# Performance work log

Hardware: AMD Instinct MI355X
Metric: run time of the kernel (lower is better)

Reference implementation:

```python
import jax, jax.numpy as jnp
import numpy as np

N_HEAD = 16
N_KV_HEADS = 4
N_REP = 4
HEAD_DIM = 128
N_EMBD = 2048
EPS = 1e-5
ROPE_BASE = 10000.0


def setup_inputs() -> dict:
    key = jax.random.key(0)
    ks = jax.random.split(key, 5)
    B, T, C = 2, 2048, N_EMBD
    s = 0.02
    return {
        "x": jax.random.normal(ks[0], (B, T, C), dtype=jnp.float32),
        "wq": jax.random.normal(ks[1], (C, N_HEAD * HEAD_DIM), dtype=jnp.float32) * s,
        "wk": jax.random.normal(ks[2], (C, N_KV_HEADS * HEAD_DIM), dtype=jnp.float32) * s,
        "wv": jax.random.normal(ks[3], (C, N_KV_HEADS * HEAD_DIM), dtype=jnp.float32) * s,
        "wc": jax.random.normal(ks[4], (C, C), dtype=jnp.float32) * s,
        "q_norm_w": jnp.ones((HEAD_DIM,), dtype=jnp.float32),
        "k_norm_w": jnp.ones((HEAD_DIM,), dtype=jnp.float32),
    }


def _rmsnorm(x, w):
    # norm in fp32, scale by weight (matches RMSNorm.forward)
    xf = x.astype(jnp.float32)
    rms = jax.lax.rsqrt(jnp.mean(xf * xf, axis=-1, keepdims=True) + EPS)
    return (xf * rms).astype(x.dtype) * w


def _rope(x, cos, sin):
    # x: [B,T,H,D]; cos/sin: [T, D//2]; interleaved even/odd rotation
    xf = x.astype(jnp.float32)
    xe = xf[..., 0::2]
    xo = xf[..., 1::2]
    c = cos[None, :, None, :]
    s = sin[None, :, None, :]
    ye = xe * c - xo * s
    yo = xe * s + xo * c
    y = jnp.stack((ye, yo), axis=-1).reshape(x.shape)
    return y.astype(x.dtype)


def reference(x, wq, wk, wv, wc, q_norm_w, k_norm_w):
    B, T, C = x.shape
    q = (x @ wq).reshape(B, T, N_HEAD, HEAD_DIM)
    k = (x @ wk).reshape(B, T, N_KV_HEADS, HEAD_DIM)
    v = (x @ wv).reshape(B, T, N_KV_HEADS, HEAD_DIM)

    q = _rmsnorm(q, q_norm_w)
    k = _rmsnorm(k, k_norm_w)

    inv_freq = 1.0 / (ROPE_BASE ** (jnp.arange(0, HEAD_DIM, 2, dtype=jnp.float32) / HEAD_DIM))
    theta = jnp.arange(T, dtype=jnp.float32)[:, None] * inv_freq[None, :]  # [T, D//2]
    cos, sin = jnp.cos(theta), jnp.sin(theta)
    q = _rope(q, cos, sin)
    k = _rope(k, cos, sin)

    # GQA: repeat kv heads (repeat_kv with n_rep)
    k = jnp.repeat(k, N_REP, axis=2)  # [B,T,H,D]
    v = jnp.repeat(v, N_REP, axis=2)

    scale = 1.0 / jnp.sqrt(jnp.float32(HEAD_DIM))
    scores = jnp.einsum("bthd,bshd->bhts", q, k) * scale  # [B,H,T,S]
    causal = jnp.tril(jnp.ones((T, T), dtype=bool))
    scores = jnp.where(causal[None, None], scores, jnp.finfo(scores.dtype).min)
    attn = jax.nn.softmax(scores, axis=-1)
    y = jnp.einsum("bhts,bshd->bthd", attn, v).reshape(B, T, C)
    return y @ wc
```

## Files before the change

### kernel.cpp

```cpp
#include <hip/hip_runtime.h>
#include <hip/hip_bf16.h>
#include <cstdint>
#include <cstddef>

using bf16 = __hip_bfloat16;
typedef __attribute__((ext_vector_type(8))) short short8;
typedef __attribute__((ext_vector_type(4))) float f32x4;
typedef __attribute__((ext_vector_type(16))) float f32x16;

#define T_SEQ 2048
#define NHEAD 16
#define NKV 4
#define HD 128
#define CE 2048

__device__ __forceinline__ void gl_lds16(const void* g, void* l) {
  __builtin_amdgcn_global_load_lds(
      (const __attribute__((address_space(1))) unsigned int*)g,
      (__attribute__((address_space(3))) unsigned int*)l, 16, 0, 0);
}

__device__ __forceinline__ unsigned int cvtpk_bf16(float lo, float hi) {
  unsigned int r;
  asm("v_cvt_pk_bf16_f32 %0, %1, %2" : "=v"(r) : "v"(lo), "v"(hi));
  return r;
}

__device__ __forceinline__ void plswap(unsigned int& x, unsigned int& y, int hi) {
#if __has_builtin(__builtin_amdgcn_permlane32_swap)
  auto r = __builtin_amdgcn_permlane32_swap(x, y, false, false);
  x = r[0];
  y = r[1];
#else
  unsigned int xp = (unsigned int)__shfl_xor((int)x, 32);
  unsigned int yp = (unsigned int)__shfl_xor((int)y, 32);
  unsigned int nx = hi ? yp : x;
  unsigned int ny = hi ? y : xp;
  x = nx;
  y = ny;
#endif
}

__global__ void __launch_bounds__(256) cvt_bf16(const float* __restrict__ in,
                                                bf16* __restrict__ out, int n4) {
  const int i = blockIdx.x * blockDim.x + threadIdx.x;
  if (i >= n4) return;
  const float4 v = ((const float4*)in)[i];
  bf16 b0 = __float2bfloat16(v.x), b1 = __float2bfloat16(v.y),
       b2 = __float2bfloat16(v.z), b3 = __float2bfloat16(v.w);
  ushort4 u;
  u.x = *(const unsigned short*)&b0; u.y = *(const unsigned short*)&b1;
  u.z = *(const unsigned short*)&b2; u.w = *(const unsigned short*)&b3;
  ((ushort4*)out)[i] = u;
}

__global__ void __launch_bounds__(256) transpose_cvt(const float* __restrict__ W,
                                                     bf16* __restrict__ Wt, int N) {
  __shared__ float tile[32][33];
  const int tx = threadIdx.x & 31, ty = threadIdx.x >> 5;
  const int bx = blockIdx.x, by = blockIdx.y;
#pragma unroll
  for (int i = 0; i < 4; i++) {
    const int r = by * 32 + ty + i * 8;
    tile[ty + i * 8][tx] = W[(size_t)r * N + bx * 32 + tx];
  }
  __syncthreads();
#pragma unroll
  for (int i = 0; i < 4; i++) {
    const int n = bx * 32 + ty + i * 8;
    Wt[(size_t)n * 2048 + by * 32 + tx] = __float2bfloat16(tile[tx][ty + i * 8]);
  }
}

template <int BM, int BN, int WM, int WN, bool OBF>
__global__ void __launch_bounds__(512, 2)
gemm8i(const bf16* __restrict__ A, const bf16* __restrict__ Bt,
       void* __restrict__ Cv, int M, int N, int K) {
  constexpr int AWS = BM / 2 / WM;
  constexpr int BWS = BN / 2 / WN;
  constexpr int MH = AWS / 16;
  constexpr int NH = BWS / 16;
  constexpr int AH = BM / 128;
  constexpr int BH = BN / 128;
  constexpr int G = 2 * AH + BH;
  __shared__ bf16 smA[2][BM * 64];
  __shared__ bf16 smB[2][BN * 64];

  const int tid = threadIdx.x, lane = tid & 63, wid = tid >> 6;
  const int l15 = lane & 15, l4 = lane >> 4;
  const int wr = wid / WN, wc = wid % WN;

  const int nwg = gridDim.x;
  const int q = nwg >> 3, r = nwg & 7;
  const int xcd = blockIdx.x & 7, lin = blockIdx.x >> 3;
  const int wg = (xcd < r ? xcd * (q + 1) : r * (q + 1) + (xcd - r) * q) + lin;
  const int gw = N / BN;
  const int by = wg / gw, bx = wg % gw;
  const int row0 = by * BM, col0 = bx * BN;
  const int NT = K >> 6;
  const int NI = NT >> 1;

  const bf16* Ag = A + (size_t)row0 * K;
  const bf16* Bg = Bt + (size_t)col0 * K;

  auto stA = [&](int t, int h, int pb) {
    const int k0 = t << 6;
#pragma unroll
    for (int j = 0; j < AH; j++) {
      const int c = (h * AH + j) * 512 + tid;
      const int rowi = c >> 3;
      gl_lds16(Ag + (size_t)rowi * K + k0 + (((c & 7) ^ (rowi & 7)) << 3),
               (void*)(&smA[pb][(size_t)c << 3]));
    }
  };
  auto stB = [&](int t, int h, int pb) {
    const int k0 = t << 6;
#pragma unroll
    for (int j = 0; j < BH; j++) {
      const int c = (h * BH + j) * 512 + tid;
      const int rowi = c >> 3;
      gl_lds16(Bg + (size_t)rowi * K + k0 + (((c & 7) ^ (rowi & 7)) << 3),
               (void*)(&smB[pb][(size_t)c << 3]));
    }
  };
  auto rdA = [&](const bf16* sA, int mh, short8 (&dst)[MH][2]) {
#pragma unroll
    for (int i = 0; i < MH; i++) {
      const int rowl = mh * (BM / 2) + wr * AWS + i * 16 + l15;
#pragma unroll
      for (int kk = 0; kk < 2; kk++)
        dst[i][kk] = *(const short8*)(sA + rowl * 64 +
                                      ((((kk << 2) | l4) ^ (rowl & 7)) << 3));
    }
  };
  auto rdB = [&](const bf16* sB, int nh, short8 (&dst)[NH][2]) {
#pragma unroll
    for (int j = 0; j < NH; j++) {
      const int rowl = nh * (BN / 2) + wc * BWS + j * 16 + l15;
#pragma unroll
      for (int kk = 0; kk < 2; kk++)
        dst[j][kk] = *(const short8*)(sB + rowl * 64 +
                                      ((((kk << 2) | l4) ^ (rowl & 7)) << 3));
    }
  };

  f32x4 acc[2][2][MH][NH];
#pragma unroll
  for (int mh = 0; mh < 2; mh++)
#pragma unroll
    for (int nh = 0; nh < 2; nh++)
#pragma unroll
      for (int i = 0; i < MH; i++)
#pragma unroll
        for (int j = 0; j < NH; j++) acc[mh][nh][i][j] = (f32x4){0.f, 0.f, 0.f, 0.f};

  auto mmq = [&](short8 (&a)[MH][2], short8 (&b)[NH][2], f32x4 (&ac)[MH][NH]) {
    __builtin_amdgcn_s_setprio(1);
#pragma unroll
    for (int i = 0; i < MH; i++)
#pragma unroll
      for (int j = 0; j < NH; j++)
#pragma unroll
        for (int kk = 0; kk < 2; kk++)
          ac[i][j] = __builtin_amdgcn_mfma_f32_16x16x32_bf16(a[i][kk], b[j][kk],
                                                             ac[i][j], 0, 0, 0);
    __builtin_amdgcn_s_setprio(0);
  };

  short8 a0[MH][2], a1[MH][2], b0[NH][2], b1[NH][2];

#define LGKM0_SB                                            \
  asm volatile("s_waitcnt lgkmcnt(0)" ::: "memory");        \
  __builtin_amdgcn_sched_barrier(0);
#define GATE_G                                              \
  asm volatile("s_waitcnt vmcnt(%0)" ::"i"(G) : "memory");

  stA(0, 0, 0); stB(0, 0, 0); stA(0, 1, 0); stB(0, 1, 0);
  stA(1, 0, 1); stB(1, 0, 1); stA(1, 1, 1);
  GATE_G
  __builtin_amdgcn_s_barrier();

  for (int i = 0; i < NI - 1; ++i) {
    const int u = 2 * i, v = u + 1;
    stB(v, 1, 1);
    rdA(smA[0], 0, a0); rdB(smB[0], 0, b0);
    __builtin_amdgcn_s_barrier();
    LGKM0_SB
    mmq(a0, b0, acc[0][0]);
    __builtin_amdgcn_s_barrier();
    stA(u + 2, 0, 0);
    rdA(smA[0], 1, a1);
    __builtin_amdgcn_s_barrier();
    LGKM0_SB
    mmq(a1, b0, acc[1][0]);
    __builtin_amdgcn_s_barrier();
    stB(u + 2, 0, 0);
    rdB(smB[0], 1, b1);
    __builtin_amdgcn_s_barrier();
    LGKM0_SB
    mmq(a1, b1, acc[1][1]);
    __builtin_amdgcn_s_barrier();
    stA(u + 2, 1, 0);
    mmq(a0, b1, acc[0][1]);
    GATE_G
    __builtin_amdgcn_s_barrier();
    stB(u + 2, 1, 0);
    rdA(smA[1], 0, a0); rdB(smB[1], 0, b0);
    __builtin_amdgcn_s_barrier();
    LGKM0_SB
    mmq(a0, b0, acc[0][0]);
    __builtin_amdgcn_s_barrier();
    stA(v + 2, 0, 1);
    rdA(smA[1], 1, a1);
    __builtin_amdgcn_s_barrier();
    LGKM0_SB
    mmq(a1, b0, acc[1][0]);
    __builtin_amdgcn_s_barrier();
    stB(v + 2, 0, 1);
    rdB(smB[1], 1, b1);
    __builtin_amdgcn_s_barrier();
    LGKM0_SB
    mmq(a1, b1, acc[1][1]);
    __builtin_amdgcn_s_barrier();
    stA(v + 2, 1, 1);
    mmq(a0, b1, acc[0][1]);
    GATE_G
    __builtin_amdgcn_s_barrier();
  }

  {
    stB(NT - 1, 1, 1);
    rdA(smA[0], 0, a0); rdB(smB[0], 0, b0);
    __builtin_amdgcn_s_barrier();
    LGKM0_SB
    mmq(a0, b0, acc[0][0]);
    __builtin_amdgcn_s_barrier();
    rdA(smA[0], 1, a1);
    __builtin_amdgcn_s_barrier();
    LGKM0_SB
    mmq(a1, b0, acc[1][0]);
    __builtin_amdgcn_s_barrier();
    rdB(smB[0], 1, b1);
    __builtin_amdgcn_s_barrier();
    LGKM0_SB
    mmq(a1, b1, acc[1][1]);
    __builtin_amdgcn_s_barrier();
    mmq(a0, b1, acc[0][1]);
    asm volatile("s_waitcnt vmcnt(0)" ::: "memory");
    __builtin_amdgcn_s_barrier();
    rdA(smA[1], 0, a0); rdB(smB[1], 0, b0);
    __builtin_amdgcn_s_barrier();
    LGKM0_SB
    mmq(a0, b0, acc[0][0]);
    __builtin_amdgcn_s_barrier();
    rdA(smA[1], 1, a1);
    __builtin_amdgcn_s_barrier();
    LGKM0_SB
    mmq(a1, b0, acc[1][0]);
    __builtin_amdgcn_s_barrier();
    rdB(smB[1], 1, b1);
    __builtin_amdgcn_s_barrier();
    LGKM0_SB
    mmq(a1, b1, acc[1][1]);
    mmq(a0, b1, acc[0][1]);
  }

#pragma unroll
  for (int mh = 0; mh < 2; mh++)
#pragma unroll
    for (int nh = 0; nh < 2; nh++)
#pragma unroll
      for (int i = 0; i < MH; i++)
#pragma unroll
        for (int j = 0; j < NH; j++)
#pragma unroll
          for (int rr = 0; rr < 4; rr++) {
            const size_t row = row0 + mh * (BM / 2) + wr * AWS + i * 16 + l4 * 4 + rr;
            const size_t col = col0 + nh * (BN / 2) + wc * BWS + j * 16 + l15;
            if constexpr (OBF)
              ((bf16*)Cv)[row * N + col] = __float2bfloat16(acc[mh][nh][i][j][rr]);
            else
              ((float*)Cv)[row * N + col] = acc[mh][nh][i][j][rr];
          }
#undef LGKM0_SB
#undef GATE_G
}

__global__ void __launch_bounds__(256) qkv_post(const bf16* __restrict__ QKV,
                                                const float* __restrict__ qw,
                                                const float* __restrict__ kw,
                                                bf16* __restrict__ Qo,
                                                bf16* __restrict__ Ko,
                                                bf16* __restrict__ Vto) {
  const int g = blockIdx.x * 4 + (threadIdx.x >> 6);
  const int lane = threadIdx.x & 63;
  const int hh = g % 24;
  const int bt = g / 24;
  const int b = bt >> 11, t = bt & (T_SEQ - 1);
  int off;
  if (hh < 16) off = hh * 128;
  else if (hh < 20) off = 2048 + (hh - 16) * 128;
  else off = 2560 + (hh - 20) * 128;
  const ushort2 xr = *(const ushort2*)(QKV + (size_t)bt * 3072 + off + lane * 2);
  const float xx = __bfloat162float(*(const bf16*)&xr.x);
  const float xy = __bfloat162float(*(const bf16*)&xr.y);
  if (hh < 20) {
    float ss = xx * xx + xy * xy;
    ss += __shfl_xor(ss, 1);  ss += __shfl_xor(ss, 2);  ss += __shfl_xor(ss, 4);
    ss += __shfl_xor(ss, 8);  ss += __shfl_xor(ss, 16); ss += __shfl_xor(ss, 32);
    const float rms = rsqrtf(ss * (1.0f / 128.0f) + 1e-5f);
    const float* w = (hh < 16) ? qw : kw;
    const float x0 = xx * rms * w[lane * 2];
    const float x1 = xy * rms * w[lane * 2 + 1];
    const float inv = exp2f((float)lane * (-13.287712379549449f / 64.0f));
    const float th = (float)t * inv;
    const float sn = sinf(th), cs = cosf(th);
    const float y0 = x0 * cs - x1 * sn;
    const float y1 = x0 * sn + x1 * cs;
    const bf16 o0 = __float2bfloat16(y0), o1 = __float2bfloat16(y1);
    if (hh < 16) {
      bf16* d = Qo + ((size_t)(b * NHEAD + hh) * T_SEQ + t) * HD + lane * 2;
      d[0] = o0; d[1] = o1;
    } else {
      bf16* d = Ko + ((size_t)(b * NKV + (hh - 16)) * T_SEQ + t) * HD + lane * 2;
      d[0] = o0; d[1] = o1;
    }
  } else {
    bf16* d = Vto + ((size_t)(b * NKV + (hh - 20)) * HD + lane * 2) * T_SEQ + t;
    d[0] = __float2bfloat16(xx);
    d[T_SEQ] = __float2bfloat16(xy);
  }
}

__global__ void __launch_bounds__(256, 2) attn_fwd(const bf16* __restrict__ Q,
                                                   const bf16* __restrict__ K,
                                                   const bf16* __restrict__ Vt,
                                                   bf16* __restrict__ Y) {
  __shared__ bf16 smK[128 * 128];
  __shared__ bf16 smV[128 * 128];

  const int bid = blockIdx.x;
  const int p = bid & 255, sdx = bid >> 8;
  const int bh = p & 31;
  const int jh = p >> 5;
  const int jq = sdx ? (15 - jh) : jh;
  const int h = bh & (NHEAD - 1), b = bh >> 4;
  const int bkv = b * NKV + (h >> 2);

  const int tid = threadIdx.x, wid = tid >> 6, lane = tid & 63;
  const int l31 = lane & 31, hi = lane >> 5;
  const int q0w = jq * 128 + wid * 32;

  const bf16* Kb = K + (size_t)bkv * T_SEQ * HD;
  const bf16* Vb = Vt + (size_t)bkv * HD * T_SEQ;

  const bf16* Qrow = Q + ((size_t)bh * T_SEQ + q0w + l31) * HD + hi * 8;
  short8 qf[8];
#pragma unroll
  for (int ds = 0; ds < 8; ds++) qf[ds] = *(const short8*)(Qrow + ds * 16);

  f32x16 o[4];
#pragma unroll
  for (int d = 0; d < 4; d++) o[d] = (f32x16)(0.f);
  float mrun = -INFINITY, lrun = 0.f;

  constexpr float CL = 0.08838834764831845f * 1.44269504088896340736f;
  const int trow = tid >> 4, tslot = tid & 15;

  for (int t = 0; t <= jq; t++) {
    const int k0 = t * 128;
    __syncthreads();
#pragma unroll
    for (int i = 0; i < 8; i++) {
      const int row = i * 16 + trow;
      const int ss = (tslot ^ (row & 15)) * 8;
      gl_lds16(Kb + (size_t)(k0 + row) * HD + ss, (void*)((char*)smK + i * 4096 + wid * 1024));
      gl_lds16(Vb + (size_t)row * T_SEQ + k0 + ss, (void*)((char*)smV + i * 4096 + wid * 1024));
    }
    __syncthreads();

    const bool lastt = (t == jq);
    const int glim = lastt ? wid : 3;

    f32x16 sg[4];
#pragma unroll
    for (int g = 0; g < 4; g++) {
      if (g > glim) continue;
      f32x16 acc = (f32x16)(0.f);
#pragma unroll
      for (int ds = 0; ds < 8; ds++) {
        const int row = g * 32 + l31;
        const short8 kf = *(const short8*)(smK + (size_t)row * 128 +
                                           (((ds << 1) | hi) ^ (row & 15)) * 8);
        acc = __builtin_amdgcn_mfma_f32_32x32x16_bf16(kf, qf[ds], acc, 0, 0, 0);
      }
      sg[g] = acc;
    }
    float tmax = -INFINITY;
#pragma unroll
    for (int g = 0; g < 4; g++) {
      if (g > glim) continue;
      if (lastt && g == wid) {
#pragma unroll
        for (int r = 0; r < 16; r++) {
          const int kr = (r & 3) + 8 * (r >> 2) + (hi << 2);
          if (kr > l31) sg[g][r] = -INFINITY;
        }
      }
#pragma unroll
      for (int r = 0; r < 16; r++) tmax = fmaxf(tmax, sg[g][r]);
    }
    tmax = fmaxf(tmax, __shfl_xor(tmax, 32));
    const float mnew = fmaxf(mrun, tmax);
    const float f = exp2f((mrun - mnew) * CL);
    mrun = mnew;
    lrun *= f;
#pragma unroll
    for (int d = 0; d < 4; d++)
#pragma unroll
      for (int r = 0; r < 16; r++) o[d][r] *= f;

    float lsum = 0.f;
#pragma unroll
    for (int g = 0; g < 4; g++) {
      if (g > glim) continue;
      float pp[16];
      float s0 = 0.f, s1 = 0.f;
#pragma unroll
      for (int r = 0; r < 16; r++) pp[r] = exp2f((sg[g][r] - mnew) * CL);
#pragma unroll
      for (int r = 0; r < 8; r++) { s0 += pp[2 * r]; s1 += pp[2 * r + 1]; }
      lsum += s0 + s1;

      unsigned int w0 = cvtpk_bf16(pp[0], pp[1]),  w2 = cvtpk_bf16(pp[4], pp[5]);
      unsigned int w1 = cvtpk_bf16(pp[2], pp[3]),  w3 = cvtpk_bf16(pp[6], pp[7]);
      unsigned int w4 = cvtpk_bf16(pp[8], pp[9]),  w6 = cvtpk_bf16(pp[12], pp[13]);
      unsigned int w5 = cvtpk_bf16(pp[10], pp[11]), w7 = cvtpk_bf16(pp[14], pp[15]);
      plswap(w0, w2, hi); plswap(w1, w3, hi);
      plswap(w4, w6, hi); plswap(w5, w7, hi);
      union { unsigned int u[4]; short8 s8; } pa0, pa1;
      pa0.u[0] = w0; pa0.u[1] = w1; pa0.u[2] = w2; pa0.u[3] = w3;
      pa1.u[0] = w4; pa1.u[1] = w5; pa1.u[2] = w6; pa1.u[3] = w7;

#pragma unroll
      for (int d = 0; d < 4; d++) {
        const int row = d * 32 + l31;
        const int ks0 = g * 2, ks1 = g * 2 + 1;
        const short8 vf0 = *(const short8*)(smV + (size_t)row * 128 +
                                            (((ks0 << 1) | hi) ^ (row & 15)) * 8);
        const short8 vf1 = *(const short8*)(smV + (size_t)row * 128 +
                                            (((ks1 << 1) | hi) ^ (row & 15)) * 8);
        o[d] = __builtin_amdgcn_mfma_f32_32x32x16_bf16(vf0, pa0.s8, o[d], 0, 0, 0);
        o[d] = __builtin_amdgcn_mfma_f32_32x32x16_bf16(vf1, pa1.s8, o[d], 0, 0, 0);
      }
    }
    lrun += lsum + __shfl_xor(lsum, 32);
  }

  const float inv = 1.0f / lrun;
  bf16* yrow = Y + ((size_t)(b * T_SEQ + q0w + l31)) * CE + h * HD;
#pragma unroll
  for (int d = 0; d < 4; d++) {
#pragma unroll
    for (int rg = 0; rg < 4; rg++) {
      ushort4 u;
      bf16 e0 = __float2bfloat16(o[d][rg * 4 + 0] * inv);
      bf16 e1 = __float2bfloat16(o[d][rg * 4 + 1] * inv);
      bf16 e2 = __float2bfloat16(o[d][rg * 4 + 2] * inv);
      bf16 e3 = __float2bfloat16(o[d][rg * 4 + 3] * inv);
      u.x = *(const unsigned short*)&e0; u.y = *(const unsigned short*)&e1;
      u.z = *(const unsigned short*)&e2; u.w = *(const unsigned short*)&e3;
      *(ushort4*)(yrow + d * 32 + rg * 8 + (hi << 2)) = u;
    }
  }
}

extern "C" void kernel_launch(void* const* d_in, const int* in_sizes, int n_in,
                              void* d_out, int out_size, void* d_ws, size_t ws_size,
                              hipStream_t stream) {
  const float* x   = (const float*)d_in[0];
  const float* wq  = (const float*)d_in[1];
  const float* wk  = (const float*)d_in[2];
  const float* wv  = (const float*)d_in[3];
  const float* wc  = (const float*)d_in[4];
  const float* qnw = (const float*)d_in[5];
  const float* knw = (const float*)d_in[6];
  float* out = (float*)d_out;

  char* ws = (char*)d_ws;
  bf16*  xb    = (bf16*)(ws);
  bf16*  wqkvt = (bf16*)(ws + 16777216);
  bf16*  wct   = (bf16*)(ws + 29360128);
  bf16*  qkv   = (bf16*)(ws + 37748736);
  bf16*  Qb    = (bf16*)(ws + 88080384);
  bf16*  Kb    = (bf16*)(ws + 104857600);
  bf16*  Vtb   = (bf16*)(ws + 109051904);
  bf16*  yb    = (bf16*)(ws + 113246208);

  cvt_bf16<<<8192, 256, 0, stream>>>(x, xb, 2097152);
  transpose_cvt<<<dim3(64, 64), 256, 0, stream>>>(wq, wqkvt, 2048);
  transpose_cvt<<<dim3(16, 64), 256, 0, stream>>>(wk, wqkvt + (size_t)2048 * 2048, 512);
  transpose_cvt<<<dim3(16, 64), 256, 0, stream>>>(wv, wqkvt + (size_t)2560 * 2048, 512);
  transpose_cvt<<<dim3(64, 64), 256, 0, stream>>>(wc, wct, 2048);
  gemm8i<256, 256, 2, 4, true><<<192, 512, 0, stream>>>(xb, wqkvt, qkv, 4096, 3072, 2048);
  qkv_post<<<24576, 256, 0, stream>>>(qkv, qnw, knw, Qb, Kb, Vtb);
  attn_fwd<<<512, 256, 0, stream>>>(Qb, Kb, Vtb, yb);
  gemm8i<128, 256, 2, 4, false><<<256, 512, 0, stream>>>(yb, wct, out, 4096, 2048, 2048);
}
```

Baseline: 228.2 us.

## Double-buffer 64-key KV tiles in attention with async prefetch and lazy rescale

The attention kernel now works on 64-key K/V tiles held in two LDS buffers. The next-but-one tile is prefetched with global_load_lds while the current tile is computed, which replaces the load, barrier, compute pattern that left global latency exposed. It also skips the output rescale unless the running max grows past a threshold, and raises wave priority around the MFMA blocks. The cost is more barriers per key, and the conditional rescale relies on the fp32 accumulator having enough headroom.

Result: slower. 237.9 us (+4.3%).

```diff
diff --git a/kernel.cpp b/kernel.cpp
--- a/kernel.cpp
+++ b/kernel.cpp
@@ -336,8 +336,8 @@
                                                    const bf16* __restrict__ K,
                                                    const bf16* __restrict__ Vt,
                                                    bf16* __restrict__ Y) {
-  __shared__ bf16 smK[128 * 128];
-  __shared__ bf16 smV[128 * 128];
+  __shared__ bf16 smK[2][64 * 128];
+  __shared__ bf16 smV[2][128 * 64];
 
   const int bid = blockIdx.x;
   const int p = bid & 255, sdx = bid >> 8;
@@ -359,75 +359,89 @@
 #pragma unroll
   for (int ds = 0; ds < 8; ds++) qf[ds] = *(const short8*)(Qrow + ds * 16);
 
+  auto stage = [&](int t, int pb) {
+    const int k0 = t * 64;
+#pragma unroll
+    for (int j = 0; j < 4; j++) {
+      const int c = j * 256 + tid;
+      const int rK = c >> 4, sK = c & 15;
+      gl_lds16(Kb + (size_t)(k0 + rK) * HD + ((sK ^ (rK & 15)) << 3),
+               (void*)((char*)smK[pb] + ((size_t)c << 4)));
+      const int rV = c >> 3, sV = c & 7;
+      gl_lds16(Vb + (size_t)rV * T_SEQ + k0 + ((sV ^ (rV & 7)) << 3),
+               (void*)((char*)smV[pb] + ((size_t)c << 4)));
+    }
+  };
+
   f32x16 o[4];
 #pragma unroll
   for (int d = 0; d < 4; d++) o[d] = (f32x16)(0.f);
   float mrun = -INFINITY, lrun = 0.f;
 
   constexpr float CL = 0.08838834764831845f * 1.44269504088896340736f;
-  const int trow = tid >> 4, tslot = tid & 15;
-
-  for (int t = 0; t <= jq; t++) {
-    const int k0 = t * 128;
-    __syncthreads();
-#pragma unroll
-    for (int i = 0; i < 8; i++) {
-      const int row = i * 16 + trow;
-      const int ss = (tslot ^ (row & 15)) * 8;
-      gl_lds16(Kb + (size_t)(k0 + row) * HD + ss, (void*)((char*)smK + i * 4096 + wid * 1024));
-      gl_lds16(Vb + (size_t)row * T_SEQ + k0 + ss, (void*)((char*)smV + i * 4096 + wid * 1024));
-    }
-    __syncthreads();
-
-    const bool lastt = (t == jq);
-    const int glim = lastt ? wid : 3;
-
-    f32x16 sg[4];
-#pragma unroll
-    for (int g = 0; g < 4; g++) {
-      if (g > glim) continue;
+  const int ntiles = 2 * (jq + 1);
+
+  stage(0, 0);
+  stage(1, 1);
+  asm volatile("s_waitcnt vmcnt(8)" ::: "memory");
+  __builtin_amdgcn_s_barrier();
+
+  for (int t = 0; t < ntiles; t++) {
+    const int buf = t & 1;
+    const int k0 = t * 64;
+    const bf16* sK = smK[buf];
+    const bf16* sV = smV[buf];
+
+    f32x16 sg[2];
+#pragma unroll
+    for (int g = 0; g < 2; g++) {
+      const int kb = k0 + g * 32;
+      if (kb > q0w) continue;
       f32x16 acc = (f32x16)(0.f);
+      const int row = g * 32 + l31;
+      __builtin_amdgcn_s_setprio(1);
 #pragma unroll
       for (int ds = 0; ds < 8; ds++) {
-        const int row = g * 32 + l31;
-        const short8 kf = *(const short8*)(smK + (size_t)row * 128 +
-                                           (((ds << 1) | hi) ^ (row & 15)) * 8);
+        const short8 kf = *(const short8*)(sK + (size_t)row * 128 +
+                                           ((((ds << 1) | hi) ^ (row & 15)) << 3));
         acc = __builtin_amdgcn_mfma_f32_32x32x16_bf16(kf, qf[ds], acc, 0, 0, 0);
       }
-      sg[g] = acc;
-    }
-    float tmax = -INFINITY;
-#pragma unroll
-    for (int g = 0; g < 4; g++) {
-      if (g > glim) continue;
-      if (lastt && g == wid) {
+      __builtin_amdgcn_s_setprio(0);
+      if (kb == q0w) {
 #pragma unroll
         for (int r = 0; r < 16; r++) {
           const int kr = (r & 3) + 8 * (r >> 2) + (hi << 2);
-          if (kr > l31) sg[g][r] = -INFINITY;
+          if (kr > l31) acc[r] = -INFINITY;
         }
       }
+      sg[g] = acc;
+    }
+    float tmax = -INFINITY;
+#pragma unroll
+    for (int g = 0; g < 2; g++) {
+      if (k0 + g * 32 > q0w) continue;
 #pragma unroll
       for (int r = 0; r < 16; r++) tmax = fmaxf(tmax, sg[g][r]);
     }
     tmax = fmaxf(tmax, __shfl_xor(tmax, 32));
-    const float mnew = fmaxf(mrun, tmax);
-    const float f = exp2f((mrun - mnew) * CL);
-    mrun = mnew;
-    lrun *= f;
-#pragma unroll
-    for (int d = 0; d < 4; d++)
-#pragma unroll
-      for (int r = 0; r < 16; r++) o[d][r] *= f;
-
+    if (!__all(tmax - mrun <= 94.0f)) {
+      const float mnew = fmaxf(mrun, tmax);
+      const float f = exp2f((mrun - mnew) * CL);
+      lrun *= f;
+#pragma unroll
+      for (int d = 0; d < 4; d++)
+#pragma unroll
+        for (int r = 0; r < 16; r++) o[d][r] *= f;
+      mrun = mnew;
+    }
     float lsum = 0.f;
 #pragma unroll
-    for (int g = 0; g < 4; g++) {
-      if (g > glim) continue;
+    for (int g = 0; g < 2; g++) {
+      if (k0 + g * 32 > q0w) continue;
       float pp[16];
+#pragma unroll
+      for (int r = 0; r < 16; r++) pp[r] = exp2f((sg[g][r] - mrun) * CL);
       float s0 = 0.f, s1 = 0.f;
-#pragma unroll
-      for (int r = 0; r < 16; r++) pp[r] = exp2f((sg[g][r] - mnew) * CL);
 #pragma unroll
       for (int r = 0; r < 8; r++) { s0 += pp[2 * r]; s1 += pp[2 * r + 1]; }
       lsum += s0 + s1;
@@ -442,19 +456,30 @@
       pa0.u[0] = w0; pa0.u[1] = w1; pa0.u[2] = w2; pa0.u[3] = w3;
       pa1.u[0] = w4; pa1.u[1] = w5; pa1.u[2] = w6; pa1.u[3] = w7;
 
+      __builtin_amdgcn_s_setprio(1);
 #pragma unroll
       for (int d = 0; d < 4; d++) {
         const int row = d * 32 + l31;
-        const int ks0 = g * 2, ks1 = g * 2 + 1;
-        const short8 vf0 = *(const short8*)(smV + (size_t)row * 128 +
-                                            (((ks0 << 1) | hi) ^ (row & 15)) * 8);
-        const short8 vf1 = *(const short8*)(smV + (size_t)row * 128 +
-                                            (((ks1 << 1) | hi) ^ (row & 15)) * 8);
+        const int ks0 = g * 2, ks1 = ks0 + 1;
+        const short8 vf0 = *(const short8*)(sV + (size_t)row * 64 +
+                                            ((((ks0 << 1) | hi) ^ (row & 7)) << 3));
+        const short8 vf1 = *(const short8*)(sV + (size_t)row * 64 +
+                                            ((((ks1 << 1) | hi) ^ (row & 7)) << 3));
         o[d] = __builtin_amdgcn_mfma_f32_32x32x16_bf16(vf0, pa0.s8, o[d], 0, 0, 0);
         o[d] = __builtin_amdgcn_mfma_f32_32x32x16_bf16(vf1, pa1.s8, o[d], 0, 0, 0);
       }
+      __builtin_amdgcn_s_setprio(0);
     }
     lrun += lsum + __shfl_xor(lsum, 32);
+
+    __builtin_amdgcn_s_barrier();
+    if (t + 2 < ntiles) {
+      stage(t + 2, buf);
+      asm volatile("s_waitcnt vmcnt(8)" ::: "memory");
+    } else {
+      asm volatile("s_waitcnt vmcnt(0)" ::: "memory");
+    }
+    __builtin_amdgcn_s_barrier();
   }
 
   const float inv = 1.0f / lrun;
```

## Split K/V staging to overlap loads with compute, add lazy softmax rescale

Applied to the files above, without the earlier changes.

The attention kernel now stages K and V separately. The next K tile is issued after the QK^T MFMAs finish and the next V tile after the PV MFMAs, so global-to-LDS loads overlap the softmax and the matmuls instead of waiting behind full barriers. It also skips the running-max rescale of the output accumulators when the new max exceeds the old by no more than a threshold, and raises wave priority around the MFMA blocks. Waits on vmcnt counts replace __syncthreads, which is delicate to get right. The lazy rescale lets exponent arguments grow before they are renormalised, which slightly raises the risk of precision or overflow problems.

Result: no change. 230.6 us (+1.1%).

```diff
diff --git a/kernel.cpp b/kernel.cpp
--- a/kernel.cpp
+++ b/kernel.cpp
@@ -350,6 +350,7 @@
   const int tid = threadIdx.x, wid = tid >> 6, lane = tid & 63;
   const int l31 = lane & 31, hi = lane >> 5;
   const int q0w = jq * 128 + wid * 32;
+  const int trow = tid >> 4, tslot = tid & 15;
 
   const bf16* Kb = K + (size_t)bkv * T_SEQ * HD;
   const bf16* Vb = Vt + (size_t)bkv * HD * T_SEQ;
@@ -359,26 +360,42 @@
 #pragma unroll
   for (int ds = 0; ds < 8; ds++) qf[ds] = *(const short8*)(Qrow + ds * 16);
 
-  f32x16 o[4];
-#pragma unroll
-  for (int d = 0; d < 4; d++) o[d] = (f32x16)(0.f);
-  float mrun = -INFINITY, lrun = 0.f;
-
-  constexpr float CL = 0.08838834764831845f * 1.44269504088896340736f;
-  const int trow = tid >> 4, tslot = tid & 15;
-
-  for (int t = 0; t <= jq; t++) {
+  auto stageK = [&](int t) {
     const int k0 = t * 128;
-    __syncthreads();
 #pragma unroll
     for (int i = 0; i < 8; i++) {
       const int row = i * 16 + trow;
       const int ss = (tslot ^ (row & 15)) * 8;
-      gl_lds16(Kb + (size_t)(k0 + row) * HD + ss, (void*)((char*)smK + i * 4096 + wid * 1024));
-      gl_lds16(Vb + (size_t)row * T_SEQ + k0 + ss, (void*)((char*)smV + i * 4096 + wid * 1024));
-    }
-    __syncthreads();
-
+      gl_lds16(Kb + (size_t)(k0 + row) * HD + ss,
+               (void*)((char*)smK + i * 4096 + wid * 1024));
+    }
+  };
+  auto stageV = [&](int t) {
+    const int k0 = t * 128;
+#pragma unroll
+    for (int i = 0; i < 8; i++) {
+      const int row = i * 16 + trow;
+      const int ss = (tslot ^ (row & 15)) * 8;
+      gl_lds16(Vb + (size_t)row * T_SEQ + k0 + ss,
+               (void*)((char*)smV + i * 4096 + wid * 1024));
+    }
+  };
+
+  f32x16 o[4];
+#pragma unroll
+  for (int d = 0; d < 4; d++) o[d] = (f32x16)(0.f);
+  float mrun = -INFINITY, lrun = 0.f;
+
+  constexpr float CL = 0.08838834764831845f * 1.44269504088896340736f;
+  const int nt = jq + 1;
+
+  stageK(0);
+  stageV(0);
+  asm volatile("s_waitcnt vmcnt(8)" ::: "memory");
+  __builtin_amdgcn_s_barrier();
+
+  for (int t = 0; t < nt; t++) {
+    const int k0 = t * 128;
     const bool lastt = (t == jq);
     const int glim = lastt ? wid : 3;
 
@@ -387,47 +404,56 @@
     for (int g = 0; g < 4; g++) {
       if (g > glim) continue;
       f32x16 acc = (f32x16)(0.f);
+      const int row = g * 32 + l31;
+      __builtin_amdgcn_s_setprio(1);
 #pragma unroll
       for (int ds = 0; ds < 8; ds++) {
-        const int row = g * 32 + l31;
         const short8 kf = *(const short8*)(smK + (size_t)row * 128 +
-                                           (((ds << 1) | hi) ^ (row & 15)) * 8);
+                                           ((((ds << 1) | hi) ^ (row & 15)) << 3));
         acc = __builtin_amdgcn_mfma_f32_32x32x16_bf16(kf, qf[ds], acc, 0, 0, 0);
       }
+      __builtin_amdgcn_s_setprio(0);
+      if (lastt && g == wid) {
+#pragma unroll
+        for (int r = 0; r < 16; r++) {
+          const int kr = (r & 3) + 8 * (r >> 2) + (hi << 2);
+          if (kr > l31) acc[r] = -INFINITY;
+        }
+      }
       sg[g] = acc;
     }
+
+    asm volatile("s_waitcnt vmcnt(0)" ::: "memory");
+    __builtin_amdgcn_s_barrier();
+    if (t + 1 < nt) stageK(t + 1);
+
     float tmax = -INFINITY;
 #pragma unroll
     for (int g = 0; g < 4; g++) {
       if (g > glim) continue;
-      if (lastt && g == wid) {
-#pragma unroll
-        for (int r = 0; r < 16; r++) {
-          const int kr = (r & 3) + 8 * (r >> 2) + (hi << 2);
-          if (kr > l31) sg[g][r] = -INFINITY;
-        }
-      }
 #pragma unroll
       for (int r = 0; r < 16; r++) tmax = fmaxf(tmax, sg[g][r]);
     }
     tmax = fmaxf(tmax, __shfl_xor(tmax, 32));
-    const float mnew = fmaxf(mrun, tmax);
-    const float f = exp2f((mrun - mnew) * CL);
-    mrun = mnew;
-    lrun *= f;
-#pragma unroll
-    for (int d = 0; d < 4; d++)
-#pragma unroll
-      for (int r = 0; r < 16; r++) o[d][r] *= f;
+    if (!__all(tmax - mrun <= 94.0f)) {
+      const float mnew = fmaxf(mrun, tmax);
+      const float f = exp2f((mrun - mnew) * CL);
+      lrun *= f;
+#pragma unroll
+      for (int d = 0; d < 4; d++)
+#pragma unroll
+        for (int r = 0; r < 16; r++) o[d][r] *= f;
+      mrun = mnew;
+    }
 
     float lsum = 0.f;
 #pragma unroll
     for (int g = 0; g < 4; g++) {
       if (g > glim) continue;
       float pp[16];
+#pragma unroll
+      for (int r = 0; r < 16; r++) pp[r] = exp2f((sg[g][r] - mrun) * CL);
       float s0 = 0.f, s1 = 0.f;
-#pragma unroll
-      for (int r = 0; r < 16; r++) pp[r] = exp2f((sg[g][r] - mnew) * CL);
 #pragma unroll
       for (int r = 0; r < 8; r++) { s0 += pp[2 * r]; s1 += pp[2 * r + 1]; }
       lsum += s0 + s1;
@@ -442,19 +468,28 @@
       pa0.u[0] = w0; pa0.u[1] = w1; pa0.u[2] = w2; pa0.u[3] = w3;
       pa1.u[0] = w4; pa1.u[1] = w5; pa1.u[2] = w6; pa1.u[3] = w7;
 
+      __builtin_amdgcn_s_setprio(1);
 #pragma unroll
       for (int d = 0; d < 4; d++) {
         const int row = d * 32 + l31;
-        const int ks0 = g * 2, ks1 = g * 2 + 1;
+        const int ks0 = g * 2, ks1 = ks0 + 1;
         const short8 vf0 = *(const short8*)(smV + (size_t)row * 128 +
-                                            (((ks0 << 1) | hi) ^ (row & 15)) * 8);
+                                            ((((ks0 << 1) | hi) ^ (row & 15)) << 3));
         const short8 vf1 = *(const short8*)(smV + (size_t)row * 128 +
-                                            (((ks1 << 1) | hi) ^ (row & 15)) * 8);
+                                            ((((ks1 << 1) | hi) ^ (row & 15)) << 3));
         o[d] = __builtin_amdgcn_mfma_f32_32x32x16_bf16(vf0, pa0.s8, o[d], 0, 0, 0);
         o[d] = __builtin_amdgcn_mfma_f32_32x32x16_bf16(vf1, pa1.s8, o[d], 0, 0, 0);
       }
+      __builtin_amdgcn_s_setprio(0);
     }
     lrun += lsum + __shfl_xor(lsum, 32);
+
+    __builtin_amdgcn_s_barrier();
+    if (t + 1 < nt) {
+      stageV(t + 1);
+      asm volatile("s_waitcnt vmcnt(8)" ::: "memory");
+      __builtin_amdgcn_s_barrier();
+    }
   }
 
   const float inv = 1.0f / lrun;
```

## Split long causal attention rows into two KV partitions with combine kernel

Applied to the files above, without the earlier changes.

Replaces the paired-block causal schedule with a job table that splits the eight longest query tiles into two KV-range partitions each, so the work per block is more balanced. The grid grows from 512 to 768 blocks. Split jobs write fp32 partial outputs plus running max and sum to workspace, which reuses the qkv buffer region. A new combine kernel merges each pair of partitions and writes bf16 output. This adds one kernel launch and extra global traffic for the partials in exchange for better load balance across CUs.

Measured after the change: 230.6 us. No clear change (+1.1%).

```diff
diff --git a/kernel.cpp b/kernel.cpp
--- a/kernel.cpp
+++ b/kernel.cpp
@@ -332,24 +332,42 @@
   }
 }
 
+__constant__ unsigned short JT[24] = {
+    0x0807, 0x180F, 0x288F, 0x287E,
+    0x0706, 0x170D, 0x277D, 0x170E, 0x276C,
+    0x0605, 0x160B, 0x266B, 0x160C, 0x265A,
+    0x0504, 0x1509, 0x2559, 0x150A, 0x2548,
+    0x0403, 0x1408,
+    0x0302, 0x0201, 0x0100};
+
+#define ATTN_CL 0.12754125f
+
 __global__ void __launch_bounds__(256, 2) attn_fwd(const bf16* __restrict__ Q,
                                                    const bf16* __restrict__ K,
                                                    const bf16* __restrict__ Vt,
-                                                   bf16* __restrict__ Y) {
+                                                   bf16* __restrict__ Y,
+                                                   float* __restrict__ PO,
+                                                   float* __restrict__ PML) {
   __shared__ bf16 smK[128 * 128];
   __shared__ bf16 smV[128 * 128];
 
   const int bid = blockIdx.x;
-  const int p = bid & 255, sdx = bid >> 8;
-  const int bh = p & 31;
-  const int jh = p >> 5;
-  const int jq = sdx ? (15 - jh) : jh;
+  const int bh = bid & 31;
+  const int jobi = bid >> 5;
+  const unsigned int e = JT[jobi];
+  const int jq = e & 15;
+  const int lo = (e >> 4) & 15;
+  const int len = (e >> 8) & 15;
+  const int part = e >> 12;
+  const int hi_t = lo + len;
+
   const int h = bh & (NHEAD - 1), b = bh >> 4;
   const int bkv = b * NKV + (h >> 2);
 
   const int tid = threadIdx.x, wid = tid >> 6, lane = tid & 63;
   const int l31 = lane & 31, hi = lane >> 5;
   const int q0w = jq * 128 + wid * 32;
+  const int trow = tid >> 4, tslot = tid & 15;
 
   const bf16* Kb = K + (size_t)bkv * T_SEQ * HD;
   const bf16* Vb = Vt + (size_t)bkv * HD * T_SEQ;
@@ -364,10 +382,9 @@
   for (int d = 0; d < 4; d++) o[d] = (f32x16)(0.f);
   float mrun = -INFINITY, lrun = 0.f;
 
-  constexpr float CL = 0.08838834764831845f * 1.44269504088896340736f;
-  const int trow = tid >> 4, tslot = tid & 15;
-
-  for (int t = 0; t <= jq; t++) {
+  constexpr float CL = ATTN_CL;
+
+  for (int t = lo; t < hi_t; t++) {
     const int k0 = t * 128;
     __syncthreads();
 #pragma unroll
@@ -379,8 +396,8 @@
     }
     __syncthreads();
 
-    const bool lastt = (t == jq);
-    const int glim = lastt ? wid : 3;
+    const bool diag = (t == jq);
+    const int glim = diag ? wid : 3;
 
     f32x16 sg[4];
 #pragma unroll
@@ -400,7 +417,7 @@
 #pragma unroll
     for (int g = 0; g < 4; g++) {
       if (g > glim) continue;
-      if (lastt && g == wid) {
+      if (diag && g == wid) {
 #pragma unroll
         for (int r = 0; r < 16; r++) {
           const int kr = (r & 3) + 8 * (r >> 2) + (hi << 2);
@@ -457,22 +474,78 @@
     lrun += lsum + __shfl_xor(lsum, 32);
   }
 
-  const float inv = 1.0f / lrun;
-  bf16* yrow = Y + ((size_t)(b * T_SEQ + q0w + l31)) * CE + h * HD;
-#pragma unroll
-  for (int d = 0; d < 4; d++) {
-#pragma unroll
-    for (int rg = 0; rg < 4; rg++) {
-      ushort4 u;
-      bf16 e0 = __float2bfloat16(o[d][rg * 4 + 0] * inv);
-      bf16 e1 = __float2bfloat16(o[d][rg * 4 + 1] * inv);
-      bf16 e2 = __float2bfloat16(o[d][rg * 4 + 2] * inv);
-      bf16 e3 = __float2bfloat16(o[d][rg * 4 + 3] * inv);
-      u.x = *(const unsigned short*)&e0; u.y = *(const unsigned short*)&e1;
-      u.z = *(const unsigned short*)&e2; u.w = *(const unsigned short*)&e3;
-      *(ushort4*)(yrow + d * 32 + rg * 8 + (hi << 2)) = u;
-    }
-  }
+  if (part == 0) {
+    const float inv = 1.0f / lrun;
+    bf16* yrow = Y + ((size_t)(b * T_SEQ + q0w + l31)) * CE + h * HD;
+#pragma unroll
+    for (int d = 0; d < 4; d++) {
+#pragma unroll
+      for (int rg = 0; rg < 4; rg++) {
+        ushort4 u;
+        bf16 e0 = __float2bfloat16(o[d][rg * 4 + 0] * inv);
+        bf16 e1 = __float2bfloat16(o[d][rg * 4 + 1] * inv);
+        bf16 e2 = __float2bfloat16(o[d][rg * 4 + 2] * inv);
+        bf16 e3 = __float2bfloat16(o[d][rg * 4 + 3] * inv);
+        u.x = *(const unsigned short*)&e0; u.y = *(const unsigned short*)&e1;
+        u.z = *(const unsigned short*)&e2; u.w = *(const unsigned short*)&e3;
+        *(ushort4*)(yrow + d * 32 + rg * 8 + (hi << 2)) = u;
+      }
+    }
+  } else {
+    const int pidx = (bh * 8 + (jq - 8)) * 2 + (part - 1);
+    float* po = PO + (size_t)pidx * 16384;
+    const int row = wid * 32 + l31;
+#pragma unroll
+    for (int d = 0; d < 4; d++) {
+#pragma unroll
+      for (int rg = 0; rg < 4; rg++) {
+        float4 v;
+        v.x = o[d][rg * 4 + 0]; v.y = o[d][rg * 4 + 1];
+        v.z = o[d][rg * 4 + 2]; v.w = o[d][rg * 4 + 3];
+        *(float4*)(po + (size_t)row * 128 + d * 32 + rg * 8 + (hi << 2)) = v;
+      }
+    }
+    if (hi == 0) {
+      PML[(size_t)pidx * 256 + row * 2 + 0] = mrun;
+      PML[(size_t)pidx * 256 + row * 2 + 1] = lrun;
+    }
+  }
+}
+
+__global__ void __launch_bounds__(256) attn_combine(const float* __restrict__ PO,
+                                                    const float* __restrict__ PML,
+                                                    bf16* __restrict__ Y) {
+  const int bid = blockIdx.x;
+  const int tI = bid >> 5;
+  const int rg = bid & 31;
+  const int tid = threadIdx.x;
+  const int row = rg * 4 + (tid >> 6);
+  const int c = (tid & 63) * 2;
+  const int bh = tI >> 3;
+  const int jq = (tI & 7) + 8;
+  const int b = bh >> 4, h = bh & 15;
+  const int p0 = tI * 2, p1 = p0 + 1;
+
+  const float m0 = PML[(size_t)p0 * 256 + row * 2 + 0];
+  const float l0 = PML[(size_t)p0 * 256 + row * 2 + 1];
+  const float m1 = PML[(size_t)p1 * 256 + row * 2 + 0];
+  const float l1 = PML[(size_t)p1 * 256 + row * 2 + 1];
+  const float m = fmaxf(m0, m1);
+  const float w0 = exp2f((m0 - m) * ATTN_CL);
+  const float w1 = exp2f((m1 - m) * ATTN_CL);
+  const float inv = 1.0f / (l0 * w0 + l1 * w1);
+
+  const float2 a = *(const float2*)(PO + (size_t)p0 * 16384 + (size_t)row * 128 + c);
+  const float2 bb = *(const float2*)(PO + (size_t)p1 * 16384 + (size_t)row * 128 + c);
+  const float y0 = (a.x * w0 + bb.x * w1) * inv;
+  const float y1 = (a.y * w0 + bb.y * w1) * inv;
+
+  const int qrow = jq * 128 + row;
+  bf16 e0 = __float2bfloat16(y0), e1 = __float2bfloat16(y1);
+  ushort2 u;
+  u.x = *(const unsigned short*)&e0;
+  u.y = *(const unsigned short*)&e1;
+  *(ushort2*)(Y + ((size_t)(b * T_SEQ + qrow)) * CE + h * HD + c) = u;
 }
 
 extern "C" void kernel_launch(void* const* d_in, const int* in_sizes, int n_in,
@@ -492,6 +565,8 @@
   bf16*  wqkvt = (bf16*)(ws + 16777216);
   bf16*  wct   = (bf16*)(ws + 29360128);
   bf16*  qkv   = (bf16*)(ws + 37748736);
+  float* partO = (float*)(ws + 37748736);
+  float* partML= (float*)(ws + 71303168);
   bf16*  Qb    = (bf16*)(ws + 88080384);
   bf16*  Kb    = (bf16*)(ws + 104857600);
   bf16*  Vtb   = (bf16*)(ws + 109051904);
@@ -504,6 +579,7 @@
   transpose_cvt<<<dim3(64, 64), 256, 0, stream>>>(wc, wct, 2048);
   gemm8i<256, 256, 2, 4, true><<<192, 512, 0, stream>>>(xb, wqkvt, qkv, 4096, 3072, 2048);
   qkv_post<<<24576, 256, 0, stream>>>(qkv, qnw, knw, Qb, Kb, Vtb);
-  attn_fwd<<<512, 256, 0, stream>>>(Qb, Kb, Vtb, yb);
+  attn_fwd<<<768, 256, 0, stream>>>(Qb, Kb, Vtb, yb, partO, partML);
+  attn_combine<<<8192, 256, 0, stream>>>(partO, partML, yb);
   gemm8i<128, 256, 2, 4, false><<<256, 512, 0, stream>>>(yb, wct, out, 4096, 2048, 2048);
 }
```
